# Kernel tuning notes

Hardware: AMD Instinct MI355X
Metric: run time of the kernel (lower is better)

Reference implementation:

```python
import jax, jax.numpy as jnp
import numpy as np

HEADS = 4
N_NODES = 20000
N_EDGES = 320000
D_IN = 128
D_HID = 128
D_EDG = 256  # = 2 * D_HID
D_OUT = 86
EPS = 1e-5
NEG_SLOPE = 0.2


def _bn(x, w, b):
    # F.batch_norm with training=True: batch statistics, biased variance
    mu = x.mean(axis=0)
    var = x.var(axis=0)
    return (x - mu) * jax.lax.rsqrt(var + EPS) * w + b


def _gat_conv(x, src, dst, W, b, a_src, a_dst):
    # multi-head GAT, head-mean output (+ bias), no self-loops
    N = x.shape[0]
    h = (x @ W.T).reshape(N, HEADS, -1)            # [N, H, D]
    alpha_s = (h * a_src).sum(-1)                  # [N, H]
    alpha_d = (h * a_dst).sum(-1)                  # [N, H]
    e = jax.nn.leaky_relu(alpha_s[src] + alpha_d[dst], NEG_SLOPE)  # [E, H]
    # segment softmax over destination neighborhoods
    m = jax.ops.segment_max(e, dst, num_segments=N)
    m = jnp.where(jnp.isfinite(m), m, 0.0)
    ex = jnp.exp(e - m[dst])
    s = jax.ops.segment_sum(ex, dst, num_segments=N)
    alpha = ex / (s[dst] + 1e-16)                  # [E, H]
    msg = alpha[:, :, None] * h[src]               # [E, H, D]
    out = jax.ops.segment_sum(msg, dst, num_segments=N)  # [N, H, D]
    return out.mean(axis=1) + b                    # [N, D]


def setup_inputs() -> dict:
    key = jax.random.key(0)
    ks = jax.random.split(key, 32)
    kn = lambda i, shape, fan: jax.random.normal(ks[i], shape, jnp.float32) * np.sqrt(2.0 / fan)
    inp = {
        "x": jax.random.normal(ks[0], (N_NODES, D_IN), jnp.float32),
        "edge_index": jax.random.randint(ks[1], (2, N_EDGES), 0, N_NODES, jnp.int32),
        # GAT layer 1
        "w0": kn(2, (D_HID * HEADS, D_IN), D_IN),
        "b0": jnp.zeros((D_HID,), jnp.float32),
        "att_src": kn(3, (1, HEADS, D_HID), D_HID),
        "att_dst": kn(4, (1, HEADS, D_HID), D_HID),
        "w1": jnp.ones((D_HID,), jnp.float32),
        "b1": jnp.zeros((D_HID,), jnp.float32),
        # GAT layer 2
        "w2": kn(5, (D_HID * HEADS, D_HID), D_HID),
        "b2": jnp.zeros((D_HID,), jnp.float32),
        "att_src1": kn(6, (1, HEADS, D_HID), D_HID),
        "att_dst1": kn(7, (1, HEADS, D_HID), D_HID),
        "w3": jnp.ones((D_HID,), jnp.float32),
        "b3": jnp.zeros((D_HID,), jnp.float32),
        # edge MLP
        "w4": kn(8, (D_EDG, D_EDG), D_EDG),
        "b4": jnp.zeros((D_EDG,), jnp.float32),
        "w5": jnp.ones((D_EDG,), jnp.float32),
        "b5": jnp.zeros((D_EDG,), jnp.float32),
        "w6": kn(9, (D_EDG, D_EDG), D_EDG),
        "b6": jnp.zeros((D_EDG,), jnp.float32),
        "w7": jnp.ones((D_EDG,), jnp.float32),
        "b7": jnp.zeros((D_EDG,), jnp.float32),
        "w8": kn(10, (D_OUT, D_EDG), D_EDG),
        "b8": jnp.zeros((D_OUT,), jnp.float32),
    }
    return inp


def reference(x, edge_index, w0, b0, att_src, att_dst, w1, b1,
              w2, b2, att_src1, att_dst1, w3, b3,
              w4, b4, w5, b5, w6, b6, w7, b7, w8, b8):
    src, dst = edge_index[0], edge_index[1]
    h = _gat_conv(x, src, dst, w0, b0, att_src, att_dst)
    h = _bn(h, w1, b1)
    x1 = jax.nn.relu(h)
    h = _gat_conv(x1, src, dst, w2, b2, att_src1, att_dst1)
    h = _bn(h, w3, b3)
    h = jax.nn.relu(h + x1)
    # edge MLP
    edge_feat = jnp.concatenate([h[src], h[dst]], axis=1)   # [E, 2*D_HID]
    edge_feat = edge_feat @ w4.T + b4
    edge_feat = jax.nn.relu(_bn(edge_feat, w5, b5))
    edge_feat = edge_feat @ w6.T + b6
    edge_feat = jax.nn.relu(_bn(edge_feat, w7, b7))
    rel_pre = edge_feat @ w8.T + b8                         # [E, D_OUT]
    return rel_pre
```

## Files before the change

### kernel.cpp

```cpp
#include <hip/hip_runtime.h>

#define NN 20000
#define NE 320000

using f32x4  = __attribute__((ext_vector_type(4))) float;
using bf16x8 = __attribute__((ext_vector_type(8))) short;

__device__ __forceinline__ float bf2f(unsigned short u){
  return __uint_as_float(((unsigned int)u) << 16);
}
__device__ __forceinline__ unsigned short f2bf(float f){
  unsigned int x = __float_as_uint(f);
  unsigned int r = ((x >> 16) & 1u) + 0x7FFFu;
  return (unsigned short)((x + r) >> 16);
}
__device__ __forceinline__ f32x4 mfma_bf16(bf16x8 a, bf16x8 b, f32x4 c){
  return __builtin_amdgcn_mfma_f32_16x16x32_bf16(a, b, c, 0, 0, 0);
}

__global__ __launch_bounds__(64)
void pack_w_k(const float* __restrict__ W, unsigned short* __restrict__ out,
              int N, int K, int mode){
  int lane = threadIdx.x;
  int KS = K >> 5;
  int nt = blockIdx.x / KS, ks = blockIdx.x % KS;
  int row = nt*16 + (lane & 15);
  int kb  = ks*32 + ((lane >> 4) << 3);
  size_t ob = ((size_t)(nt*KS + ks)*64 + lane)*8;
  #pragma unroll
  for(int i=0;i<8;i++){
    int k = kb + i; float f = 0.f;
    if(row < N){
      f = (mode == 0) ? W[(size_t)row*K + k]
        : (row < 256 ? W[(size_t)row*256 + k] : W[(size_t)(row-256)*256 + 128 + k]);
    }
    out[ob + i] = f2bf(f);
  }
}

template<int NT, int KS, bool FUSE, bool ALPHA>
__global__ __launch_bounds__(256)
void gemm_node_k(const float* __restrict__ A, const unsigned short* __restrict__ Bp,
                 unsigned short* __restrict__ C, const float* __restrict__ sc,
                 const float* __restrict__ sh, const float* __restrict__ res,
                 const float* __restrict__ att_s, const float* __restrict__ att_d,
                 float* __restrict__ as_, float* __restrict__ ad_,
                 int M, int K, int N){
  int lane = threadIdx.x & 63, w = threadIdx.x >> 6;
  int rowbase = blockIdx.x*64 + w*16;
  int nt0 = blockIdx.y * NT;
  f32x4 acc[NT];
  #pragma unroll
  for(int i=0;i<NT;i++) acc[i] = (f32x4){0.f,0.f,0.f,0.f};
  int arow = rowbase + (lane & 15); if(arow > M-1) arow = M-1;
  const float* ap = A + (size_t)arow*K + ((lane >> 4) << 3);
  const float* rp = FUSE ? (res + (size_t)arow*K + ((lane >> 4) << 3)) : nullptr;
  const bf16x8* bp = (const bf16x8*)Bp;
  #pragma unroll
  for(int ks=0; ks<KS; ks++){
    int k0 = ks*32 + ((lane >> 4) << 3);
    f32x4 a0 = *(const f32x4*)(ap + ks*32);
    f32x4 a1 = *(const f32x4*)(ap + ks*32 + 4);
    bf16x8 af;
    if constexpr (FUSE){
      f32x4 c0 = *(const f32x4*)(sc + k0), c1 = *(const f32x4*)(sc + k0 + 4);
      f32x4 h0 = *(const f32x4*)(sh + k0), h1 = *(const f32x4*)(sh + k0 + 4);
      f32x4 r0 = *(const f32x4*)(rp + ks*32), r1 = *(const f32x4*)(rp + ks*32 + 4);
      #pragma unroll
      for(int i=0;i<4;i++){
        af[i]   = (short)f2bf(fmaxf(a0[i]*c0[i] + h0[i] + r0[i], 0.f));
        af[i+4] = (short)f2bf(fmaxf(a1[i]*c1[i] + h1[i] + r1[i], 0.f));
      }
    } else {
      #pragma unroll
      for(int i=0;i<4;i++){ af[i] = (short)f2bf(a0[i]); af[i+4] = (short)f2bf(a1[i]); }
    }
    #pragma unroll
    for(int nt=0; nt<NT; nt++)
      acc[nt] = mfma_bf16(af, bp[((size_t)(nt0+nt)*KS + ks)*64 + lane], acc[nt]);
  }
  #pragma unroll
  for(int nt=0; nt<NT; nt++){
    int col = (nt0+nt)*16 + (lane & 15);
    #pragma unroll
    for(int r=0;r<4;r++){
      int row = rowbase + ((lane >> 4) << 2) + r;
      if(row < M) C[(size_t)row*N + col] = f2bf(acc[nt][r]);
    }
  }
  if constexpr (ALPHA){
    float ps[2][4] = {{0.f,0.f,0.f,0.f},{0.f,0.f,0.f,0.f}};
    float pd[2][4] = {{0.f,0.f,0.f,0.f},{0.f,0.f,0.f,0.f}};
    #pragma unroll
    for(int nt=0; nt<NT; nt++){
      int col = (nt0+nt)*16 + (lane & 15);
      float sv = att_s[col], dv = att_d[col];
      int hh = (col >> 7) & 1;
      #pragma unroll
      for(int r=0;r<4;r++){ ps[hh][r] += acc[nt][r]*sv; pd[hh][r] += acc[nt][r]*dv; }
    }
    #pragma unroll
    for(int m=1;m<16;m<<=1){
      #pragma unroll
      for(int hh=0;hh<2;hh++){
        #pragma unroll
        for(int r=0;r<4;r++){
          ps[hh][r] += __shfl_xor(ps[hh][r], m);
          pd[hh][r] += __shfl_xor(pd[hh][r], m);
        }
      }
    }
    if((lane & 15) == 0){
      int h0 = nt0 >> 3;
      #pragma unroll
      for(int r=0;r<4;r++){
        int row = rowbase + ((lane >> 4) << 2) + r;
        if(row < M){
          #pragma unroll
          for(int hh=0;hh<2;hh++){
            as_[row*4 + h0 + hh] = ps[hh][r];
            ad_[row*4 + h0 + hh] = pd[hh][r];
          }
        }
      }
    }
  }
}

__global__ __launch_bounds__(256)
void edge_e_k(const float* __restrict__ as_, const float* __restrict__ ad_,
              const int* __restrict__ esrc, const int* __restrict__ edst,
              const int* __restrict__ epos, float* __restrict__ ebuf){
  int e = blockIdx.x*256 + threadIdx.x; if(e >= NE) return;
  f32x4 a = *(const f32x4*)(as_ + (size_t)esrc[e]*4);
  f32x4 b = *(const f32x4*)(ad_ + (size_t)edst[e]*4);
  f32x4 v;
  #pragma unroll
  for(int h=0;h<4;h++){ float t = a[h] + b[h]; v[h] = t > 0.f ? t : 0.2f*t; }
  *(f32x4*)(ebuf + (size_t)epos[e]*4) = v;
}

__global__ __launch_bounds__(256)
void hist_k(const int* __restrict__ edst, int* __restrict__ cnt){
  int e = blockIdx.x*256 + threadIdx.x; if(e >= NE) return;
  atomicAdd(&cnt[edst[e]], 1);
}
__global__ __launch_bounds__(1024)
void scan_k(const int* __restrict__ cnt, int* __restrict__ rowp, int n){
  __shared__ int part[1024];
  int t = threadIdx.x, base = t*20;
  int s = 0;
  for(int j=0;j<20;j++) if(base+j < n) s += cnt[base+j];
  part[t] = s;
  for(int off=1; off<1024; off<<=1){
    __syncthreads();
    int u = (t >= off) ? part[t-off] : 0;
    __syncthreads();
    part[t] += u;
  }
  __syncthreads();
  int run = part[t] - s;
  for(int j=0;j<20;j++){ int idx = base+j; if(idx < n){ rowp[idx] = run; run += cnt[idx]; } }
  if(t == 1023) rowp[n] = part[1023];
}
__global__ __launch_bounds__(256)
void scatter_k(const int* __restrict__ esrc, const int* __restrict__ edst,
               const int* __restrict__ rowp, int* __restrict__ cnt2,
               int* __restrict__ eids, int* __restrict__ esrc_csr,
               int* __restrict__ edst_csr, int* __restrict__ epos){
  int e = blockIdx.x*256 + threadIdx.x; if(e >= NE) return;
  int d = edst[e];
  int pos = atomicAdd(&cnt2[d], 1);
  int j = rowp[d] + pos;
  eids[j] = e;
  esrc_csr[j] = esrc[e];
  edst_csr[j] = d;
  epos[e] = j;
}

__global__ __launch_bounds__(256)
void gat_aggregate_k(const unsigned short* __restrict__ hbuf, const float* __restrict__ ebuf,
                     const int* __restrict__ rowp, const int* __restrict__ esrc_csr,
                     const float* __restrict__ bias, float* __restrict__ outn, int nN){
  int lane = threadIdx.x & 63, w = threadIdx.x >> 6;
  int node = blockIdx.x*4 + w; if(node >= nN) return;
  int start = rowp[node], end = rowp[node+1];
  int h = lane >> 4, jl = lane & 15;
  float m = -1e30f;
  for(int j = start + jl; j < end; j += 16) m = fmaxf(m, ebuf[(size_t)j*4 + h]);
  #pragma unroll
  for(int msk=1; msk<16; msk<<=1) m = fmaxf(m, __shfl_xor(m, msk));
  float s = 0.f;
  for(int j = start + jl; j < end; j += 16) s += expf(ebuf[(size_t)j*4 + h] - m);
  #pragma unroll
  for(int msk=1; msk<16; msk<<=1) s += __shfl_xor(s, msk);
  float inv = 1.f/(s + 1e-16f);
  float acc[8] = {0.f,0.f,0.f,0.f,0.f,0.f,0.f,0.f};
  int j = start;
  for(; j + 4 <= end; j += 4){
    int s0 = esrc_csr[j],   s1 = esrc_csr[j+1];
    int s2 = esrc_csr[j+2], s3 = esrc_csr[j+3];
    float e0 = ebuf[(size_t)j*4 + h],     e1 = ebuf[(size_t)(j+1)*4 + h];
    float e2 = ebuf[(size_t)(j+2)*4 + h], e3 = ebuf[(size_t)(j+3)*4 + h];
    bf16x8 v0 = *(const bf16x8*)(hbuf + (size_t)s0*512 + lane*8);
    bf16x8 v1 = *(const bf16x8*)(hbuf + (size_t)s1*512 + lane*8);
    bf16x8 v2 = *(const bf16x8*)(hbuf + (size_t)s2*512 + lane*8);
    bf16x8 v3 = *(const bf16x8*)(hbuf + (size_t)s3*512 + lane*8);
    float a0 = expf(e0 - m)*inv, a1 = expf(e1 - m)*inv;
    float a2 = expf(e2 - m)*inv, a3 = expf(e3 - m)*inv;
    #pragma unroll
    for(int i=0;i<8;i++)
      acc[i] += a0*bf2f((unsigned short)v0[i]) + a1*bf2f((unsigned short)v1[i])
              + a2*bf2f((unsigned short)v2[i]) + a3*bf2f((unsigned short)v3[i]);
  }
  for(; j < end; j++){
    int sa = esrc_csr[j];
    float aa = expf(ebuf[(size_t)j*4 + h] - m)*inv;
    bf16x8 va = *(const bf16x8*)(hbuf + (size_t)sa*512 + lane*8);
    #pragma unroll
    for(int i=0;i<8;i++) acc[i] += aa*bf2f((unsigned short)va[i]);
  }
  #pragma unroll
  for(int i=0;i<8;i++){ acc[i] += __shfl_xor(acc[i], 16); acc[i] += __shfl_xor(acc[i], 32); }
  if(lane < 16){
    #pragma unroll
    for(int i=0;i<8;i++)
      outn[(size_t)node*128 + lane*8 + i] = acc[i]*0.25f + bias[lane*8 + i];
  }
}

__global__ __launch_bounds__(256)
void bn_stats_k(const float* __restrict__ X, float* __restrict__ sum,
                float* __restrict__ sq, int M){
  int tid = threadIdx.x; int c = tid & 127;
  float s = 0.f, q = 0.f;
  for(int r = blockIdx.x*2 + (tid>>7); r < M; r += 512){
    float v = X[(size_t)r*128 + c]; s += v; q += v*v;
  }
  __shared__ float S[256], Q[256];
  S[tid] = s; Q[tid] = q; __syncthreads();
  if(tid < 128){ atomicAdd(&sum[c], S[tid]+S[tid+128]); atomicAdd(&sq[c], Q[tid]+Q[tid+128]); }
}

__global__ __launch_bounds__(256)
void bn_finalize_k(const float* __restrict__ sum, const float* __restrict__ sq, float count,
                   const float* __restrict__ wbn, const float* __restrict__ bbn,
                   const float* __restrict__ badd, float* __restrict__ A,
                   float* __restrict__ B, int C){
  int c = blockIdx.x*256 + threadIdx.x; if(c >= C) return;
  float mu = sum[c]/count;
  float var = sq[c]/count - mu*mu;
  float a = rsqrtf(var + 1e-5f) * wbn[c];
  float ba = badd ? badd[c] : 0.f;
  A[c] = a; B[c] = (ba - mu)*a + bbn[c];
}

template<bool RES>
__global__ __launch_bounds__(256)
void bn_apply_k(const float* __restrict__ in, const float* __restrict__ A,
                const float* __restrict__ B, const float* __restrict__ res,
                float* __restrict__ out, int total){
  int i = blockIdx.x*256 + threadIdx.x; if(i >= total) return;
  int c = i & 127;
  float v = in[i]*A[c] + B[c];
  if(RES) v += res[i];
  out[i] = fmaxf(v, 0.f);
}

__global__ __launch_bounds__(256)
void edge_stats1_k(const unsigned short* __restrict__ PQ, const int* __restrict__ esrc_csr,
                   const int* __restrict__ edst_csr, const float* __restrict__ b4,
                   float* __restrict__ s1, float* __restrict__ q1){
  int c = threadIdx.x;
  float bc = b4[c];
  float s = 0.f, q = 0.f;
  int j0 = blockIdx.x*256;
  #pragma unroll 8
  for(int j=0;j<256;j++){
    int p = j0 + j;
    int sr = esrc_csr[p], dn = edst_csr[p];
    float v = bf2f(PQ[(size_t)sr*512 + c]) + bf2f(PQ[(size_t)dn*512 + 256 + c]) + bc;
    s += v; q += v*v;
  }
  atomicAdd(&s1[c], s); atomicAdd(&q1[c], q);
}

__device__ __forceinline__ bf16x8 gather_t1_frag(const unsigned short* prow,
    const unsigned short* qrow, const float* SC1, const float* SH1, int k0){
  bf16x8 pv = *(const bf16x8*)(prow + k0);
  bf16x8 qv = *(const bf16x8*)(qrow + k0);
  f32x4 sc0 = *(const f32x4*)(SC1 + k0), sc1 = *(const f32x4*)(SC1 + k0 + 4);
  f32x4 sh0 = *(const f32x4*)(SH1 + k0), sh1 = *(const f32x4*)(SH1 + k0 + 4);
  bf16x8 af;
  #pragma unroll
  for(int i=0;i<4;i++){
    float t = bf2f((unsigned short)pv[i])   + bf2f((unsigned short)qv[i]);
    t = fmaxf(t*sc0[i] + sh0[i], 0.f);
    af[i] = (short)f2bf(t);
    float u = bf2f((unsigned short)pv[i+4]) + bf2f((unsigned short)qv[i+4]);
    u = fmaxf(u*sc1[i] + sh1[i], 0.f);
    af[i+4] = (short)f2bf(u);
  }
  return af;
}

template<bool STORE>
__global__ __launch_bounds__(256)
void edge_gemm1_k(const unsigned short* __restrict__ PQ, const int* __restrict__ esrc_csr,
                  const int* __restrict__ edst_csr, const float* __restrict__ SC1,
                  const float* __restrict__ SH1, const unsigned short* __restrict__ w6p,
                  const float* __restrict__ b6, unsigned short* __restrict__ t2,
                  float* __restrict__ s2, float* __restrict__ q2){
  int lane = threadIdx.x & 63, w = threadIdx.x >> 6;
  int jbase = blockIdx.x*64 + w*16;
  int jr = jbase + (lane & 15);
  int sr = esrc_csr[jr], dn = edst_csr[jr];
  const unsigned short* prow = PQ + (size_t)sr*512;
  const unsigned short* qrow = PQ + (size_t)dn*512 + 256;
  f32x4 acc[16];
  #pragma unroll
  for(int i=0;i<16;i++) acc[i] = (f32x4){0.f,0.f,0.f,0.f};
  const bf16x8* bp = (const bf16x8*)w6p;
  #pragma unroll
  for(int ks=0; ks<8; ks++){
    int k0 = ks*32 + ((lane >> 4) << 3);
    bf16x8 af = gather_t1_frag(prow, qrow, SC1, SH1, k0);
    #pragma unroll
    for(int nt=0; nt<16; nt++)
      acc[nt] = mfma_bf16(af, bp[(size_t)(nt*8 + ks)*64 + lane], acc[nt]);
  }
  __shared__ float redS[4][256];
  __shared__ float redQ[4][256];
  #pragma unroll
  for(int nt=0; nt<16; nt++){
    int col = nt*16 + (lane & 15);
    float b6c = b6[col];
    f32x4 v = acc[nt];
    #pragma unroll
    for(int r=0;r<4;r++) v[r] += b6c;
    acc[nt] = v;
    float ps = v[0]+v[1]+v[2]+v[3];
    float pq = v[0]*v[0]+v[1]*v[1]+v[2]*v[2]+v[3]*v[3];
    ps += __shfl_xor(ps, 16); ps += __shfl_xor(ps, 32);
    pq += __shfl_xor(pq, 16); pq += __shfl_xor(pq, 32);
    if(lane < 16){ redS[w][col] = ps; redQ[w][col] = pq; }
  }
  if constexpr (STORE){
    #pragma unroll
    for(int nt=0; nt<16; nt++){
      int col = nt*16 + (lane & 15);
      #pragma unroll
      for(int r=0;r<4;r++){
        int row = jbase + ((lane >> 4) << 2) + r;
        t2[(size_t)row*256 + col] = f2bf(acc[nt][r]);
      }
    }
  }
  __syncthreads();
  int c = threadIdx.x;
  float ts = redS[0][c]+redS[1][c]+redS[2][c]+redS[3][c];
  float tq = redQ[0][c]+redQ[1][c]+redQ[2][c]+redQ[3][c];
  atomicAdd(&s2[c], ts); atomicAdd(&q2[c], tq);
}

__global__ __launch_bounds__(256)
void edge_gemm2_k(const unsigned short* __restrict__ t2, const int* __restrict__ eids,
                  const float* __restrict__ SC2, const float* __restrict__ SH2,
                  const unsigned short* __restrict__ w8p, const float* __restrict__ b8,
                  float* __restrict__ outp){
  int lane = threadIdx.x & 63, w = threadIdx.x >> 6;
  int ebase = blockIdx.x*64 + w*16;
  const unsigned short* arow = t2 + (size_t)(ebase + (lane & 15))*256;
  int orig[4];
  #pragma unroll
  for(int r=0;r<4;r++) orig[r] = eids[ebase + ((lane >> 4) << 2) + r];
  f32x4 acc[6];
  #pragma unroll
  for(int i=0;i<6;i++) acc[i] = (f32x4){0.f,0.f,0.f,0.f};
  const bf16x8* bp = (const bf16x8*)w8p;
  #pragma unroll
  for(int ks=0; ks<8; ks++){
    int k0 = ks*32 + ((lane >> 4) << 3);
    bf16x8 tv = *(const bf16x8*)(arow + k0);
    f32x4 sc0 = *(const f32x4*)(SC2 + k0), sc1 = *(const f32x4*)(SC2 + k0 + 4);
    f32x4 sh0 = *(const f32x4*)(SH2 + k0), sh1 = *(const f32x4*)(SH2 + k0 + 4);
    bf16x8 af;
    #pragma unroll
    for(int i=0;i<4;i++){
      float t = fmaxf(bf2f((unsigned short)tv[i])*sc0[i]   + sh0[i], 0.f);
      af[i] = (short)f2bf(t);
      float u = fmaxf(bf2f((unsigned short)tv[i+4])*sc1[i] + sh1[i], 0.f);
      af[i+4] = (short)f2bf(u);
    }
    #pragma unroll
    for(int nt=0; nt<6; nt++)
      acc[nt] = mfma_bf16(af, bp[(size_t)(nt*8 + ks)*64 + lane], acc[nt]);
  }
  #pragma unroll
  for(int nt=0; nt<6; nt++){
    int col = nt*16 + (lane & 15);
    if(col < 86){
      float bb = b8[col];
      #pragma unroll
      for(int r=0;r<4;r++)
        outp[(size_t)orig[r]*86 + col] = acc[nt][r] + bb;
    }
  }
}

__global__ __launch_bounds__(256)
void edge_fused_k(const unsigned short* __restrict__ PQ, const int* __restrict__ esrc_csr,
                  const int* __restrict__ edst_csr, const int* __restrict__ eids,
                  const float* __restrict__ SC1, const float* __restrict__ SH1,
                  const unsigned short* __restrict__ w6p, const float* __restrict__ b6,
                  const float* __restrict__ SC2, const float* __restrict__ SH2,
                  const unsigned short* __restrict__ w8p, const float* __restrict__ b8,
                  float* __restrict__ outp){
  int lane = threadIdx.x & 63, w = threadIdx.x >> 6;
  int jbase = blockIdx.x*64 + w*16;
  int jr = jbase + (lane & 15);
  int sr = esrc_csr[jr], dn = edst_csr[jr];
  int orig[4];
  #pragma unroll
  for(int r=0;r<4;r++) orig[r] = eids[jbase + ((lane >> 4) << 2) + r];
  const unsigned short* prow = PQ + (size_t)sr*512;
  const unsigned short* qrow = PQ + (size_t)dn*512 + 256;
  f32x4 acc[16];
  #pragma unroll
  for(int i=0;i<16;i++) acc[i] = (f32x4){0.f,0.f,0.f,0.f};
  const bf16x8* bp6 = (const bf16x8*)w6p;
  #pragma unroll
  for(int ks=0; ks<8; ks++){
    int k0 = ks*32 + ((lane >> 4) << 3);
    bf16x8 af = gather_t1_frag(prow, qrow, SC1, SH1, k0);
    #pragma unroll
    for(int nt=0; nt<16; nt++)
      acc[nt] = mfma_bf16(af, bp6[(size_t)(nt*8 + ks)*64 + lane], acc[nt]);
  }
  __shared__ alignas(16) unsigned short tile[4][16][264];
  #pragma unroll
  for(int nt=0; nt<16; nt++){
    int col = nt*16 + (lane & 15);
    float b6c = b6[col], sc = SC2[col], sh = SH2[col];
    #pragma unroll
    for(int r=0;r<4;r++){
      float t = fmaxf((acc[nt][r] + b6c)*sc + sh, 0.f);
      tile[w][((lane >> 4) << 2) + r][col] = f2bf(t);
    }
  }
  __syncthreads();
  f32x4 acc2[6];
  #pragma unroll
  for(int i=0;i<6;i++) acc2[i] = (f32x4){0.f,0.f,0.f,0.f};
  const bf16x8* bp8 = (const bf16x8*)w8p;
  #pragma unroll
  for(int ks=0; ks<8; ks++){
    int k0 = ks*32 + ((lane >> 4) << 3);
    bf16x8 af = *(const bf16x8*)&tile[w][lane & 15][k0];
    #pragma unroll
    for(int nt=0; nt<6; nt++)
      acc2[nt] = mfma_bf16(af, bp8[(size_t)(nt*8 + ks)*64 + lane], acc2[nt]);
  }
  #pragma unroll
  for(int nt=0; nt<6; nt++){
    int col = nt*16 + (lane & 15);
    if(col < 86){
      float bb = b8[col];
      #pragma unroll
      for(int r=0;r<4;r++)
        outp[(size_t)orig[r]*86 + col] = acc2[nt][r] + bb;
    }
  }
}

extern "C" void kernel_launch(void* const* d_in, const int* in_sizes, int n_in,
                              void* d_out, int out_size, void* d_ws, size_t ws_size,
                              hipStream_t stream){
  const float* x      = (const float*)d_in[0];
  const int*   ei     = (const int*)  d_in[1];
  const float* w0     = (const float*)d_in[2];
  const float* b0     = (const float*)d_in[3];
  const float* att_s0 = (const float*)d_in[4];
  const float* att_d0 = (const float*)d_in[5];
  const float* w1     = (const float*)d_in[6];
  const float* b1     = (const float*)d_in[7];
  const float* w2     = (const float*)d_in[8];
  const float* b2     = (const float*)d_in[9];
  const float* att_s1 = (const float*)d_in[10];
  const float* att_d1 = (const float*)d_in[11];
  const float* w3     = (const float*)d_in[12];
  const float* b3     = (const float*)d_in[13];
  const float* w4     = (const float*)d_in[14];
  const float* b4     = (const float*)d_in[15];
  const float* w5     = (const float*)d_in[16];
  const float* b5     = (const float*)d_in[17];
  const float* w6     = (const float*)d_in[18];
  const float* b6     = (const float*)d_in[19];
  const float* w7     = (const float*)d_in[20];
  const float* b7     = (const float*)d_in[21];
  const float* w8     = (const float*)d_in[22];
  const float* b8     = (const float*)d_in[23];
  float* outp = (float*)d_out;
  char* ws = (char*)d_ws;
  const int* esrc = ei;
  const int* edst = ei + NE;

  size_t cur = 0;
  auto alloc = [&](size_t bytes){ size_t o = cur; cur = (cur + bytes + 255) & ~((size_t)255); return o; };
  size_t o_hbuf = alloc((size_t)20032*512*2);
  size_t o_out1 = alloc((size_t)NN*128*4);
  size_t o_x1   = alloc((size_t)NN*128*4);
  size_t o_as   = alloc((size_t)NN*4*4);
  size_t o_ad   = alloc((size_t)NN*4*4);
  size_t o_ebuf = alloc((size_t)NE*4*4);
  size_t o_eids = alloc((size_t)NE*4);
  size_t o_escr = alloc((size_t)NE*4);
  size_t o_edcr = alloc((size_t)NE*4);
  size_t o_epos = alloc((size_t)NE*4);
  size_t o_w0p  = alloc((size_t)512*128*2);
  size_t o_w2p  = alloc((size_t)512*128*2);
  size_t o_w4p  = alloc((size_t)512*128*2);
  size_t o_w6p  = alloc((size_t)256*256*2);
  size_t o_w8p  = alloc((size_t)96*256*2);
  size_t o_rowp = alloc((size_t)(NN+1)*4);
  size_t o_nA1  = alloc(128*4); size_t o_nB1 = alloc(128*4);
  size_t o_nA2  = alloc(128*4); size_t o_nB2 = alloc(128*4);
  size_t o_SC1  = alloc(256*4); size_t o_SH1 = alloc(256*4);
  size_t o_SC2  = alloc(256*4); size_t o_SH2 = alloc(256*4);
  size_t zstart = cur;
  size_t o_cnt  = alloc((size_t)(NN+1)*4);
  size_t o_cnt2 = alloc((size_t)(NN+1)*4);
  size_t o_nS1  = alloc(128*4); size_t o_nQ1 = alloc(128*4);
  size_t o_nS2  = alloc(128*4); size_t o_nQ2 = alloc(128*4);
  size_t o_eS1  = alloc(256*4); size_t o_eQ1 = alloc(256*4);
  size_t o_eS2  = alloc(256*4); size_t o_eQ2 = alloc(256*4);
  size_t zbytes = cur - zstart;
  size_t o_t2 = cur;
  bool store_t2 = ws_size >= o_t2 + (size_t)NE*256*2;

  unsigned short* hbuf = (unsigned short*)(ws + o_hbuf);
  float* out1  = (float*)(ws + o_out1);
  float* x1b   = (float*)(ws + o_x1);
  float* asb   = (float*)(ws + o_as);
  float* adb   = (float*)(ws + o_ad);
  float* ebuf  = (float*)(ws + o_ebuf);
  int*   eids  = (int*)(ws + o_eids);
  int*   escr  = (int*)(ws + o_escr);
  int*   edcr  = (int*)(ws + o_edcr);
  int*   epos  = (int*)(ws + o_epos);
  unsigned short* w0p = (unsigned short*)(ws + o_w0p);
  unsigned short* w2p = (unsigned short*)(ws + o_w2p);
  unsigned short* w4p = (unsigned short*)(ws + o_w4p);
  unsigned short* w6p = (unsigned short*)(ws + o_w6p);
  unsigned short* w8p = (unsigned short*)(ws + o_w8p);
  int* rowp = (int*)(ws + o_rowp);
  int* cnt  = (int*)(ws + o_cnt);
  int* cnt2 = (int*)(ws + o_cnt2);
  float* nA1 = (float*)(ws+o_nA1); float* nB1 = (float*)(ws+o_nB1);
  float* nA2 = (float*)(ws+o_nA2); float* nB2 = (float*)(ws+o_nB2);
  float* SC1 = (float*)(ws+o_SC1); float* SH1 = (float*)(ws+o_SH1);
  float* SC2 = (float*)(ws+o_SC2); float* SH2 = (float*)(ws+o_SH2);
  float* nS1 = (float*)(ws+o_nS1); float* nQ1 = (float*)(ws+o_nQ1);
  float* nS2 = (float*)(ws+o_nS2); float* nQ2 = (float*)(ws+o_nQ2);
  float* eS1 = (float*)(ws+o_eS1); float* eQ1 = (float*)(ws+o_eQ1);
  float* eS2 = (float*)(ws+o_eS2); float* eQ2 = (float*)(ws+o_eQ2);
  unsigned short* t2p = (unsigned short*)(ws + o_t2);

  hipMemsetAsync(ws + zstart, 0, zbytes, stream);

  pack_w_k<<<32*4, 64, 0, stream>>>(w0, w0p, 512, 128, 0);
  pack_w_k<<<32*4, 64, 0, stream>>>(w2, w2p, 512, 128, 0);
  pack_w_k<<<32*4, 64, 0, stream>>>(w4, w4p, 512, 128, 1);
  pack_w_k<<<16*8, 64, 0, stream>>>(w6, w6p, 256, 256, 0);
  pack_w_k<<<6*8,  64, 0, stream>>>(w8, w8p,  86, 256, 0);

  hist_k   <<<1250, 256, 0, stream>>>(edst, cnt);
  scan_k   <<<1, 1024, 0, stream>>>(cnt, rowp, NN);
  scatter_k<<<1250, 256, 0, stream>>>(esrc, edst, rowp, cnt2, eids, escr, edcr, epos);

  gemm_node_k<16,4,false,true><<<dim3(313,2), 256, 0, stream>>>(
      x, w0p, hbuf, nullptr, nullptr, nullptr, att_s0, att_d0, asb, adb, NN, 128, 512);
  edge_e_k<<<1250, 256, 0, stream>>>(asb, adb, esrc, edst, epos, ebuf);
  gat_aggregate_k<<<5000, 256, 0, stream>>>(hbuf, ebuf, rowp, escr, b0, out1, NN);
  bn_stats_k<<<256, 256, 0, stream>>>(out1, nS1, nQ1, NN);
  bn_finalize_k<<<1, 256, 0, stream>>>(nS1, nQ1, (float)NN, w1, b1, nullptr, nA1, nB1, 128);
  bn_apply_k<false><<<10000, 256, 0, stream>>>(out1, nA1, nB1, nullptr, x1b, NN*128);

  gemm_node_k<16,4,false,true><<<dim3(313,2), 256, 0, stream>>>(
      x1b, w2p, hbuf, nullptr, nullptr, nullptr, att_s1, att_d1, asb, adb, NN, 128, 512);
  edge_e_k<<<1250, 256, 0, stream>>>(asb, adb, esrc, edst, epos, ebuf);
  gat_aggregate_k<<<5000, 256, 0, stream>>>(hbuf, ebuf, rowp, escr, b2, out1, NN);
  bn_stats_k<<<256, 256, 0, stream>>>(out1, nS2, nQ2, NN);
  bn_finalize_k<<<1, 256, 0, stream>>>(nS2, nQ2, (float)NN, w3, b3, nullptr, nA2, nB2, 128);

  gemm_node_k<16,4,true,false><<<dim3(313,2), 256, 0, stream>>>(
      out1, w4p, hbuf, nA2, nB2, x1b, nullptr, nullptr, nullptr, nullptr, NN, 128, 512);
  edge_stats1_k<<<1250, 256, 0, stream>>>(hbuf, escr, edcr, b4, eS1, eQ1);
  bn_finalize_k<<<1, 256, 0, stream>>>(eS1, eQ1, (float)NE, w5, b5, b4, SC1, SH1, 256);
  if(store_t2){
    edge_gemm1_k<true><<<5000, 256, 0, stream>>>(hbuf, escr, edcr, SC1, SH1, w6p, b6, t2p, eS2, eQ2);
    bn_finalize_k<<<1, 256, 0, stream>>>(eS2, eQ2, (float)NE, w7, b7, nullptr, SC2, SH2, 256);
    edge_gemm2_k<<<5000, 256, 0, stream>>>(t2p, eids, SC2, SH2, w8p, b8, outp);
  } else {
    edge_gemm1_k<false><<<5000, 256, 0, stream>>>(hbuf, escr, edcr, SC1, SH1, w6p, b6, nullptr, eS2, eQ2);
    bn_finalize_k<<<1, 256, 0, stream>>>(eS2, eQ2, (float)NE, w7, b7, nullptr, SC2, SH2, 256);
    edge_fused_k<<<5000, 256, 0, stream>>>(hbuf, escr, edcr, eids, SC1, SH1, w6p, b6, SC2, SH2, w8p, b8, outp);
  }
}
```

Before: 695.5 us.

## Materialize first edge-MLP activation once and recompute second GEMM in fused pass

Before, when workspace allowed, the code stored the second-layer pre-activation t2 and ran a separate final GEMM. Now a new kernel gathers the source and destination projections once, writes the biased first-layer pre-activation t1 as contiguous bf16 rows, and accumulates its BN statistics. Both later passes stream t1 instead of gathering rows twice. The last pass recomputes the w6 GEMM and feeds its BN+ReLU output through shared memory into the w8 GEMM, which trades extra MFMA work for dropping the t2 store and reload. BN statistics are now taken from the bf16-rounded values, so precision changes slightly.

```diff
diff --git a/kernel.cpp b/kernel.cpp
--- a/kernel.cpp
+++ b/kernel.cpp
@@ -268,6 +268,157 @@
 }
 
 __global__ __launch_bounds__(256)
+void edge_t1_k(const unsigned short* __restrict__ PQ, const int* __restrict__ esrc_csr,
+               const int* __restrict__ edst_csr, const float* __restrict__ b4,
+               unsigned short* __restrict__ t1, float* __restrict__ s1,
+               float* __restrict__ q1){
+  int tid = threadIdx.x;
+  int cp = tid & 127;
+  int eh = tid >> 7;
+  float bc0 = b4[2*cp], bc1 = b4[2*cp+1];
+  float s0 = 0.f, q0 = 0.f, s1v = 0.f, q1v = 0.f;
+  int j0 = blockIdx.x*256;
+  for(int j=0;j<128;j++){
+    int p = j0 + 2*j + eh;
+    int sr = esrc_csr[p], dn = edst_csr[p];
+    unsigned int pu = *(const unsigned int*)(PQ + (size_t)sr*512 + 2*cp);
+    unsigned int qu = *(const unsigned int*)(PQ + (size_t)dn*512 + 256 + 2*cp);
+    float v0 = bf2f((unsigned short)(pu & 0xFFFF)) + bf2f((unsigned short)(qu & 0xFFFF)) + bc0;
+    float v1 = bf2f((unsigned short)(pu >> 16))    + bf2f((unsigned short)(qu >> 16))    + bc1;
+    unsigned short r0 = f2bf(v0), r1 = f2bf(v1);
+    *(unsigned int*)(t1 + (size_t)p*256 + 2*cp) = ((unsigned int)r1 << 16) | r0;
+    float f0 = bf2f(r0), f1 = bf2f(r1);
+    s0 += f0; q0 += f0*f0; s1v += f1; q1v += f1*f1;
+  }
+  __shared__ float S0[256], Q0[256], S1[256], Q1[256];
+  S0[tid] = s0; Q0[tid] = q0; S1[tid] = s1v; Q1[tid] = q1v;
+  __syncthreads();
+  if(tid < 128){
+    atomicAdd(&s1[2*tid],   S0[tid]+S0[tid+128]);
+    atomicAdd(&q1[2*tid],   Q0[tid]+Q0[tid+128]);
+    atomicAdd(&s1[2*tid+1], S1[tid]+S1[tid+128]);
+    atomicAdd(&q1[2*tid+1], Q1[tid]+Q1[tid+128]);
+  }
+}
+
+__device__ __forceinline__ bf16x8 stream_frag(const unsigned short* arow,
+    const float* SC, const float* SH, int k0){
+  bf16x8 tv = *(const bf16x8*)(arow + k0);
+  f32x4 sc0 = *(const f32x4*)(SC + k0), sc1 = *(const f32x4*)(SC + k0 + 4);
+  f32x4 sh0 = *(const f32x4*)(SH + k0), sh1 = *(const f32x4*)(SH + k0 + 4);
+  bf16x8 af;
+  #pragma unroll
+  for(int i=0;i<4;i++){
+    af[i]   = (short)f2bf(fmaxf(bf2f((unsigned short)tv[i])*sc0[i]   + sh0[i], 0.f));
+    af[i+4] = (short)f2bf(fmaxf(bf2f((unsigned short)tv[i+4])*sc1[i] + sh1[i], 0.f));
+  }
+  return af;
+}
+
+__global__ __launch_bounds__(256)
+void edge_gemm1s_k(const unsigned short* __restrict__ t1, const float* __restrict__ SC1,
+                   const float* __restrict__ SH1, const unsigned short* __restrict__ w6p,
+                   const float* __restrict__ b6, float* __restrict__ s2,
+                   float* __restrict__ q2){
+  int lane = threadIdx.x & 63, w = threadIdx.x >> 6;
+  int jbase = blockIdx.x*64 + w*16;
+  const unsigned short* arow = t1 + (size_t)(jbase + (lane & 15))*256;
+  f32x4 acc[16];
+  #pragma unroll
+  for(int i=0;i<16;i++) acc[i] = (f32x4){0.f,0.f,0.f,0.f};
+  const bf16x8* bp = (const bf16x8*)w6p;
+  #pragma unroll
+  for(int ks=0; ks<8; ks++){
+    int k0 = ks*32 + ((lane >> 4) << 3);
+    bf16x8 af = stream_frag(arow, SC1, SH1, k0);
+    #pragma unroll
+    for(int nt=0; nt<16; nt++)
+      acc[nt] = mfma_bf16(af, bp[(size_t)(nt*8 + ks)*64 + lane], acc[nt]);
+  }
+  __shared__ float redS[4][256];
+  __shared__ float redQ[4][256];
+  #pragma unroll
+  for(int nt=0; nt<16; nt++){
+    int col = nt*16 + (lane & 15);
+    float b6c = b6[col];
+    f32x4 v = acc[nt];
+    #pragma unroll
+    for(int r=0;r<4;r++) v[r] += b6c;
+    float ps = v[0]+v[1]+v[2]+v[3];
+    float pq = v[0]*v[0]+v[1]*v[1]+v[2]*v[2]+v[3]*v[3];
+    ps += __shfl_xor(ps, 16); ps += __shfl_xor(ps, 32);
+    pq += __shfl_xor(pq, 16); pq += __shfl_xor(pq, 32);
+    if(lane < 16){ redS[w][col] = ps; redQ[w][col] = pq; }
+  }
+  __syncthreads();
+  int c = threadIdx.x;
+  float ts = redS[0][c]+redS[1][c]+redS[2][c]+redS[3][c];
+  float tq = redQ[0][c]+redQ[1][c]+redQ[2][c]+redQ[3][c];
+  atomicAdd(&s2[c], ts); atomicAdd(&q2[c], tq);
+}
+
+__global__ __launch_bounds__(256)
+void edge_fused_s_k(const unsigned short* __restrict__ t1, const int* __restrict__ eids,
+                    const float* __restrict__ SC1, const float* __restrict__ SH1,
+                    const unsigned short* __restrict__ w6p, const float* __restrict__ b6,
+                    const float* __restrict__ SC2, const float* __restrict__ SH2,
+                    const unsigned short* __restrict__ w8p, const float* __restrict__ b8,
+                    float* __restrict__ outp){
+  int lane = threadIdx.x & 63, w = threadIdx.x >> 6;
+  int jbase = blockIdx.x*64 + w*16;
+  const unsigned short* arow = t1 + (size_t)(jbase + (lane & 15))*256;
+  int orig[4];
+  #pragma unroll
+  for(int r=0;r<4;r++) orig[r] = eids[jbase + ((lane >> 4) << 2) + r];
+  f32x4 acc[16];
+  #pragma unroll
+  for(int i=0;i<16;i++) acc[i] = (f32x4){0.f,0.f,0.f,0.f};
+  const bf16x8* bp6 = (const bf16x8*)w6p;
+  #pragma unroll
+  for(int ks=0; ks<8; ks++){
+    int k0 = ks*32 + ((lane >> 4) << 3);
+    bf16x8 af = stream_frag(arow, SC1, SH1, k0);
+    #pragma unroll
+    for(int nt=0; nt<16; nt++)
+      acc[nt] = mfma_bf16(af, bp6[(size_t)(nt*8 + ks)*64 + lane], acc[nt]);
+  }
+  __shared__ alignas(16) unsigned short tile[4][16][264];
+  #pragma unroll
+  for(int nt=0; nt<16; nt++){
+    int col = nt*16 + (lane & 15);
+    float b6c = b6[col], sc = SC2[col], sh = SH2[col];
+    #pragma unroll
+    for(int r=0;r<4;r++){
+      float t = fmaxf((acc[nt][r] + b6c)*sc + sh, 0.f);
+      tile[w][((lane >> 4) << 2) + r][col] = f2bf(t);
+    }
+  }
+  __syncthreads();
+  f32x4 acc2[6];
+  #pragma unroll
+  for(int i=0;i<6;i++) acc2[i] = (f32x4){0.f,0.f,0.f,0.f};
+  const bf16x8* bp8 = (const bf16x8*)w8p;
+  #pragma unroll
+  for(int ks=0; ks<8; ks++){
+    int k0 = ks*32 + ((lane >> 4) << 3);
+    bf16x8 af = *(const bf16x8*)&tile[w][lane & 15][k0];
+    #pragma unroll
+    for(int nt=0; nt<6; nt++)
+      acc2[nt] = mfma_bf16(af, bp8[(size_t)(nt*8 + ks)*64 + lane], acc2[nt]);
+  }
+  #pragma unroll
+  for(int nt=0; nt<6; nt++){
+    int col = nt*16 + (lane & 15);
+    if(col < 86){
+      float bb = b8[col];
+      #pragma unroll
+      for(int r=0;r<4;r++)
+        outp[(size_t)orig[r]*86 + col] = acc2[nt][r] + bb;
+    }
+  }
+}
+
+__global__ __launch_bounds__(256)
 void edge_stats1_k(const unsigned short* __restrict__ PQ, const int* __restrict__ esrc_csr,
                    const int* __restrict__ edst_csr, const float* __restrict__ b4,
                    float* __restrict__ s1, float* __restrict__ q1){
@@ -295,22 +446,19 @@
   #pragma unroll
   for(int i=0;i<4;i++){
     float t = bf2f((unsigned short)pv[i])   + bf2f((unsigned short)qv[i]);
-    t = fmaxf(t*sc0[i] + sh0[i], 0.f);
-    af[i] = (short)f2bf(t);
+    af[i] = (short)f2bf(fmaxf(t*sc0[i] + sh0[i], 0.f));
     float u = bf2f((unsigned short)pv[i+4]) + bf2f((unsigned short)qv[i+4]);
-    u = fmaxf(u*sc1[i] + sh1[i], 0.f);
-    af[i+4] = (short)f2bf(u);
+    af[i+4] = (short)f2bf(fmaxf(u*sc1[i] + sh1[i], 0.f));
   }
   return af;
 }
 
-template<bool STORE>
 __global__ __launch_bounds__(256)
 void edge_gemm1_k(const unsigned short* __restrict__ PQ, const int* __restrict__ esrc_csr,
                   const int* __restrict__ edst_csr, const float* __restrict__ SC1,
                   const float* __restrict__ SH1, const unsigned short* __restrict__ w6p,
-                  const float* __restrict__ b6, unsigned short* __restrict__ t2,
-                  float* __restrict__ s2, float* __restrict__ q2){
+                  const float* __restrict__ b6, float* __restrict__ s2,
+                  float* __restrict__ q2){
   int lane = threadIdx.x & 63, w = threadIdx.x >> 6;
   int jbase = blockIdx.x*64 + w*16;
   int jr = jbase + (lane & 15);
@@ -338,74 +486,17 @@
     f32x4 v = acc[nt];
     #pragma unroll
     for(int r=0;r<4;r++) v[r] += b6c;
-    acc[nt] = v;
     float ps = v[0]+v[1]+v[2]+v[3];
     float pq = v[0]*v[0]+v[1]*v[1]+v[2]*v[2]+v[3]*v[3];
     ps += __shfl_xor(ps, 16); ps += __shfl_xor(ps, 32);
     pq += __shfl_xor(pq, 16); pq += __shfl_xor(pq, 32);
     if(lane < 16){ redS[w][col] = ps; redQ[w][col] = pq; }
   }
-  if constexpr (STORE){
-    #pragma unroll
-    for(int nt=0; nt<16; nt++){
-      int col = nt*16 + (lane & 15);
-      #pragma unroll
-      for(int r=0;r<4;r++){
-        int row = jbase + ((lane >> 4) << 2) + r;
-        t2[(size_t)row*256 + col] = f2bf(acc[nt][r]);
-      }
-    }
-  }
   __syncthreads();
   int c = threadIdx.x;
   float ts = redS[0][c]+redS[1][c]+redS[2][c]+redS[3][c];
   float tq = redQ[0][c]+redQ[1][c]+redQ[2][c]+redQ[3][c];
   atomicAdd(&s2[c], ts); atomicAdd(&q2[c], tq);
-}
-
-__global__ __launch_bounds__(256)
-void edge_gemm2_k(const unsigned short* __restrict__ t2, const int* __restrict__ eids,
-                  const float* __restrict__ SC2, const float* __restrict__ SH2,
-                  const unsigned short* __restrict__ w8p, const float* __restrict__ b8,
-                  float* __restrict__ outp){
-  int lane = threadIdx.x & 63, w = threadIdx.x >> 6;
-  int ebase = blockIdx.x*64 + w*16;
-  const unsigned short* arow = t2 + (size_t)(ebase + (lane & 15))*256;
-  int orig[4];
-  #pragma unroll
-  for(int r=0;r<4;r++) orig[r] = eids[ebase + ((lane >> 4) << 2) + r];
-  f32x4 acc[6];
-  #pragma unroll
-  for(int i=0;i<6;i++) acc[i] = (f32x4){0.f,0.f,0.f,0.f};
-  const bf16x8* bp = (const bf16x8*)w8p;
-  #pragma unroll
-  for(int ks=0; ks<8; ks++){
-    int k0 = ks*32 + ((lane >> 4) << 3);
-    bf16x8 tv = *(const bf16x8*)(arow + k0);
-    f32x4 sc0 = *(const f32x4*)(SC2 + k0), sc1 = *(const f32x4*)(SC2 + k0 + 4);
-    f32x4 sh0 = *(const f32x4*)(SH2 + k0), sh1 = *(const f32x4*)(SH2 + k0 + 4);
-    bf16x8 af;
-    #pragma unroll
-    for(int i=0;i<4;i++){
-      float t = fmaxf(bf2f((unsigned short)tv[i])*sc0[i]   + sh0[i], 0.f);
-      af[i] = (short)f2bf(t);
-      float u = fmaxf(bf2f((unsigned short)tv[i+4])*sc1[i] + sh1[i], 0.f);
-      af[i+4] = (short)f2bf(u);
-    }
-    #pragma unroll
-    for(int nt=0; nt<6; nt++)
-      acc[nt] = mfma_bf16(af, bp[(size_t)(nt*8 + ks)*64 + lane], acc[nt]);
-  }
-  #pragma unroll
-  for(int nt=0; nt<6; nt++){
-    int col = nt*16 + (lane & 15);
-    if(col < 86){
-      float bb = b8[col];
-      #pragma unroll
-      for(int r=0;r<4;r++)
-        outp[(size_t)orig[r]*86 + col] = acc[nt][r] + bb;
-    }
-  }
 }
 
 __global__ __launch_bounds__(256)
@@ -535,8 +626,8 @@
   size_t o_eS1  = alloc(256*4); size_t o_eQ1 = alloc(256*4);
   size_t o_eS2  = alloc(256*4); size_t o_eQ2 = alloc(256*4);
   size_t zbytes = cur - zstart;
-  size_t o_t2 = cur;
-  bool store_t2 = ws_size >= o_t2 + (size_t)NE*256*2;
+  size_t o_t1 = cur;
+  bool use_t1 = ws_size >= o_t1 + (size_t)NE*256*2;
 
   unsigned short* hbuf = (unsigned short*)(ws + o_hbuf);
   float* out1  = (float*)(ws + o_out1);
@@ -564,7 +655,7 @@
   float* nS2 = (float*)(ws+o_nS2); float* nQ2 = (float*)(ws+o_nQ2);
   float* eS1 = (float*)(ws+o_eS1); float* eQ1 = (float*)(ws+o_eQ1);
   float* eS2 = (float*)(ws+o_eS2); float* eQ2 = (float*)(ws+o_eQ2);
-  unsigned short* t2p = (unsigned short*)(ws + o_t2);
+  unsigned short* t1p = (unsigned short*)(ws + o_t1);
 
   hipMemsetAsync(ws + zstart, 0, zbytes, stream);
 
@@ -595,14 +686,16 @@
 
   gemm_node_k<16,4,true,false><<<dim3(313,2), 256, 0, stream>>>(
       out1, w4p, hbuf, nA2, nB2, x1b, nullptr, nullptr, nullptr, nullptr, NN, 128, 512);
-  edge_stats1_k<<<1250, 256, 0, stream>>>(hbuf, escr, edcr, b4, eS1, eQ1);
-  bn_finalize_k<<<1, 256, 0, stream>>>(eS1, eQ1, (float)NE, w5, b5, b4, SC1, SH1, 256);
-  if(store_t2){
-    edge_gemm1_k<true><<<5000, 256, 0, stream>>>(hbuf, escr, edcr, SC1, SH1, w6p, b6, t2p, eS2, eQ2);
+  if(use_t1){
+    edge_t1_k<<<1250, 256, 0, stream>>>(hbuf, escr, edcr, b4, t1p, eS1, eQ1);
+    bn_finalize_k<<<1, 256, 0, stream>>>(eS1, eQ1, (float)NE, w5, b5, nullptr, SC1, SH1, 256);
+    edge_gemm1s_k<<<5000, 256, 0, stream>>>(t1p, SC1, SH1, w6p, b6, eS2, eQ2);
     bn_finalize_k<<<1, 256, 0, stream>>>(eS2, eQ2, (float)NE, w7, b7, nullptr, SC2, SH2, 256);
-    edge_gemm2_k<<<5000, 256, 0, stream>>>(t2p, eids, SC2, SH2, w8p, b8, outp);
+    edge_fused_s_k<<<5000, 256, 0, stream>>>(t1p, eids, SC1, SH1, w6p, b6, SC2, SH2, w8p, b8, outp);
   } else {
-    edge_gemm1_k<false><<<5000, 256, 0, stream>>>(hbuf, escr, edcr, SC1, SH1, w6p, b6, nullptr, eS2, eQ2);
+    edge_stats1_k<<<1250, 256, 0, stream>>>(hbuf, escr, edcr, b4, eS1, eQ1);
+    bn_finalize_k<<<1, 256, 0, stream>>>(eS1, eQ1, (float)NE, w5, b5, b4, SC1, SH1, 256);
+    edge_gemm1_k<<<5000, 256, 0, stream>>>(hbuf, escr, edcr, SC1, SH1, w6p, b6, eS2, eQ2);
     bn_finalize_k<<<1, 256, 0, stream>>>(eS2, eQ2, (float)NE, w7, b7, nullptr, SC2, SH2, 256);
     edge_fused_k<<<5000, 256, 0, stream>>>(hbuf, escr, edcr, eids, SC1, SH1, w6p, b6, SC2, SH2, w8p, b8, outp);
   }
```

Result: slower. 1.161 ms (+67.0%).

## Stage gathered edge tile in LDS and split GEMM columns across waves

Applied to the files above, without the earlier changes.

edge_gemm1_k now gathers and normalizes the 64-edge A tile once into shared memory. Each wave then computes a 64x64 output block (4 row tiles by 4 column tiles) instead of one wave covering all 256 columns for 16 rows. This reuses each loaded weight fragment across four row tiles and cuts per-wave accumulator registers from 16 to 16 fragments with better B reuse. BN statistics now go straight to global atomics per wave instead of a shared reduction, which means more atomic traffic in exchange for dropping the LDS reduction arrays and the barrier.

```diff
diff --git a/kernel.cpp b/kernel.cpp
--- a/kernel.cpp
+++ b/kernel.cpp
@@ -285,25 +285,6 @@
   atomicAdd(&s1[c], s); atomicAdd(&q1[c], q);
 }
 
-__device__ __forceinline__ bf16x8 gather_t1_frag(const unsigned short* prow,
-    const unsigned short* qrow, const float* SC1, const float* SH1, int k0){
-  bf16x8 pv = *(const bf16x8*)(prow + k0);
-  bf16x8 qv = *(const bf16x8*)(qrow + k0);
-  f32x4 sc0 = *(const f32x4*)(SC1 + k0), sc1 = *(const f32x4*)(SC1 + k0 + 4);
-  f32x4 sh0 = *(const f32x4*)(SH1 + k0), sh1 = *(const f32x4*)(SH1 + k0 + 4);
-  bf16x8 af;
-  #pragma unroll
-  for(int i=0;i<4;i++){
-    float t = bf2f((unsigned short)pv[i])   + bf2f((unsigned short)qv[i]);
-    t = fmaxf(t*sc0[i] + sh0[i], 0.f);
-    af[i] = (short)f2bf(t);
-    float u = bf2f((unsigned short)pv[i+4]) + bf2f((unsigned short)qv[i+4]);
-    u = fmaxf(u*sc1[i] + sh1[i], 0.f);
-    af[i+4] = (short)f2bf(u);
-  }
-  return af;
-}
-
 template<bool STORE>
 __global__ __launch_bounds__(256)
 void edge_gemm1_k(const unsigned short* __restrict__ PQ, const int* __restrict__ esrc_csr,
@@ -311,56 +292,87 @@
                   const float* __restrict__ SH1, const unsigned short* __restrict__ w6p,
                   const float* __restrict__ b6, unsigned short* __restrict__ t2,
                   float* __restrict__ s2, float* __restrict__ q2){
-  int lane = threadIdx.x & 63, w = threadIdx.x >> 6;
-  int jbase = blockIdx.x*64 + w*16;
-  int jr = jbase + (lane & 15);
-  int sr = esrc_csr[jr], dn = edst_csr[jr];
-  const unsigned short* prow = PQ + (size_t)sr*512;
-  const unsigned short* qrow = PQ + (size_t)dn*512 + 256;
-  f32x4 acc[16];
-  #pragma unroll
-  for(int i=0;i<16;i++) acc[i] = (f32x4){0.f,0.f,0.f,0.f};
+  __shared__ alignas(16) unsigned short At[64][264];
+  int tid = threadIdx.x;
+  int lane = tid & 63, w = tid >> 6;
+  int jbase = blockIdx.x*64;
+  {
+    int row = tid >> 2, chunk = tid & 3, c0 = chunk*64;
+    int sr = esrc_csr[jbase + row], dn = edst_csr[jbase + row];
+    const unsigned short* prow = PQ + (size_t)sr*512 + c0;
+    const unsigned short* qrow = PQ + (size_t)dn*512 + 256 + c0;
+    unsigned short* dstp = &At[row][c0];
+    #pragma unroll
+    for(int i=0;i<8;i++){
+      bf16x8 pv = *(const bf16x8*)(prow + i*8);
+      bf16x8 qv = *(const bf16x8*)(qrow + i*8);
+      f32x4 sa = *(const f32x4*)(SC1 + c0 + i*8);
+      f32x4 sb = *(const f32x4*)(SC1 + c0 + i*8 + 4);
+      f32x4 ha = *(const f32x4*)(SH1 + c0 + i*8);
+      f32x4 hb = *(const f32x4*)(SH1 + c0 + i*8 + 4);
+      bf16x8 o;
+      #pragma unroll
+      for(int k=0;k<4;k++){
+        float t = bf2f((unsigned short)pv[k]) + bf2f((unsigned short)qv[k]);
+        o[k] = (short)f2bf(fmaxf(t*sa[k] + ha[k], 0.f));
+        float u = bf2f((unsigned short)pv[k+4]) + bf2f((unsigned short)qv[k+4]);
+        o[k+4] = (short)f2bf(fmaxf(u*sb[k] + hb[k], 0.f));
+      }
+      *(bf16x8*)(dstp + i*8) = o;
+    }
+  }
+  __syncthreads();
+  f32x4 acc[4][4];
+  #pragma unroll
+  for(int i=0;i<4;i++)
+    #pragma unroll
+    for(int j=0;j<4;j++) acc[i][j] = (f32x4){0.f,0.f,0.f,0.f};
   const bf16x8* bp = (const bf16x8*)w6p;
   #pragma unroll
   for(int ks=0; ks<8; ks++){
     int k0 = ks*32 + ((lane >> 4) << 3);
-    bf16x8 af = gather_t1_frag(prow, qrow, SC1, SH1, k0);
-    #pragma unroll
-    for(int nt=0; nt<16; nt++)
-      acc[nt] = mfma_bf16(af, bp[(size_t)(nt*8 + ks)*64 + lane], acc[nt]);
-  }
-  __shared__ float redS[4][256];
-  __shared__ float redQ[4][256];
-  #pragma unroll
-  for(int nt=0; nt<16; nt++){
-    int col = nt*16 + (lane & 15);
+    bf16x8 bfr[4];
+    #pragma unroll
+    for(int n=0;n<4;n++) bfr[n] = bp[(size_t)((4*w+n)*8 + ks)*64 + lane];
+    #pragma unroll
+    for(int rt=0;rt<4;rt++){
+      bf16x8 af = *(const bf16x8*)&At[rt*16 + (lane & 15)][k0];
+      #pragma unroll
+      for(int n=0;n<4;n++) acc[rt][n] = mfma_bf16(af, bfr[n], acc[rt][n]);
+    }
+  }
+  #pragma unroll
+  for(int n=0;n<4;n++){
+    int col = (4*w+n)*16 + (lane & 15);
     float b6c = b6[col];
-    f32x4 v = acc[nt];
-    #pragma unroll
-    for(int r=0;r<4;r++) v[r] += b6c;
-    acc[nt] = v;
-    float ps = v[0]+v[1]+v[2]+v[3];
-    float pq = v[0]*v[0]+v[1]*v[1]+v[2]*v[2]+v[3]*v[3];
+    float ps = 0.f, pq = 0.f;
+    #pragma unroll
+    for(int rt=0;rt<4;rt++){
+      f32x4 v = acc[rt][n];
+      #pragma unroll
+      for(int r=0;r<4;r++) v[r] += b6c;
+      acc[rt][n] = v;
+      ps += v[0]+v[1]+v[2]+v[3];
+      pq += v[0]*v[0]+v[1]*v[1]+v[2]*v[2]+v[3]*v[3];
+    }
     ps += __shfl_xor(ps, 16); ps += __shfl_xor(ps, 32);
     pq += __shfl_xor(pq, 16); pq += __shfl_xor(pq, 32);
-    if(lane < 16){ redS[w][col] = ps; redQ[w][col] = pq; }
+    if(lane < 16){ atomicAdd(&s2[col], ps); atomicAdd(&q2[col], pq); }
   }
   if constexpr (STORE){
     #pragma unroll
-    for(int nt=0; nt<16; nt++){
-      int col = nt*16 + (lane & 15);
-      #pragma unroll
-      for(int r=0;r<4;r++){
-        int row = jbase + ((lane >> 4) << 2) + r;
-        t2[(size_t)row*256 + col] = f2bf(acc[nt][r]);
+    for(int n=0;n<4;n++){
+      int col = (4*w+n)*16 + (lane & 15);
+      #pragma unroll
+      for(int rt=0;rt<4;rt++){
+        #pragma unroll
+        for(int r=0;r<4;r++){
+          int row = jbase + rt*16 + ((lane >> 4) << 2) + r;
+          t2[(size_t)row*256 + col] = f2bf(acc[rt][n][r]);
+        }
       }
     }
   }
-  __syncthreads();
-  int c = threadIdx.x;
-  float ts = redS[0][c]+redS[1][c]+redS[2][c]+redS[3][c];
-  float tq = redQ[0][c]+redQ[1][c]+redQ[2][c]+redQ[3][c];
-  atomicAdd(&s2[c], ts); atomicAdd(&q2[c], tq);
 }
 
 __global__ __launch_bounds__(256)
@@ -406,6 +418,23 @@
         outp[(size_t)orig[r]*86 + col] = acc[nt][r] + bb;
     }
   }
+}
+
+__device__ __forceinline__ bf16x8 gather_t1_frag(const unsigned short* prow,
+    const unsigned short* qrow, const float* SC1, const float* SH1, int k0){
+  bf16x8 pv = *(const bf16x8*)(prow + k0);
+  bf16x8 qv = *(const bf16x8*)(qrow + k0);
+  f32x4 sc0 = *(const f32x4*)(SC1 + k0), sc1 = *(const f32x4*)(SC1 + k0 + 4);
+  f32x4 sh0 = *(const f32x4*)(SH1 + k0), sh1 = *(const f32x4*)(SH1 + k0 + 4);
+  bf16x8 af;
+  #pragma unroll
+  for(int i=0;i<4;i++){
+    float t = bf2f((unsigned short)pv[i])   + bf2f((unsigned short)qv[i]);
+    af[i] = (short)f2bf(fmaxf(t*sc0[i] + sh0[i], 0.f));
+    float u = bf2f((unsigned short)pv[i+4]) + bf2f((unsigned short)qv[i+4]);
+    af[i+4] = (short)f2bf(fmaxf(u*sc1[i] + sh1[i], 0.f));
+  }
+  return af;
 }
 
 __global__ __launch_bounds__(256)
```

Result: no change. 690.3 us (-0.7%).
